# Kernel tuning notes

Measured on AMD Instinct MI355X. Metric: run time of the kernel, lower is better.

## Reference

```python
import jax, jax.numpy as jnp
import numpy as np

B, H, S, D = 2, 16, 2048, 64
MASK_NEG = 1e9


def setup_inputs() -> dict:
    key = jax.random.key(0)
    kq, kk, kv, km = jax.random.split(key, 4)
    Q = jax.random.normal(kq, (B, H, S, D), dtype=jnp.float32)
    K = jax.random.normal(kk, (B, H, S, D), dtype=jnp.float32)
    V = jax.random.normal(kv, (B, H, S, D), dtype=jnp.float32)
    # float 0/1 mask, broadcast over heads; 1 = masked-out position
    attn_mask = jax.random.randint(km, (B, 1, S, S), 0, 2).astype(jnp.float32)
    return {"Q": Q, "K": K, "V": V, "attn_mask": attn_mask}


def reference(Q, K, V, attn_mask):
    # scores: [B, H, S, S]
    attn_score = jnp.einsum('bhqd,bhkd->bhqk', Q, K)
    scale = jnp.sqrt(jnp.asarray(K.shape[-1], dtype=jnp.float32))
    attn_scale = attn_score / scale - MASK_NEG * attn_mask
    attn_prob = jax.nn.softmax(attn_scale, axis=-1)
    attn_out = jnp.einsum('bhqk,bhkd->bhqd', attn_prob, V)
    return attn_out
```

## Files before the change

kernel.cpp:

```cpp
#include <hip/hip_runtime.h>


#define S_LEN 2048
#define D_DIM 64
#define WPR   32
#define NIT   32

typedef __attribute__((ext_vector_type(8)))  short bf16x8;
typedef __attribute__((ext_vector_type(4)))  float f32x4;
typedef __attribute__((ext_vector_type(16))) float f32x16;
typedef unsigned uint2v __attribute__((ext_vector_type(2)));
typedef unsigned long long ull;

__device__ __forceinline__ f32x16 mfma32(bf16x8 a, bf16x8 b, f32x16 c) {
  return __builtin_amdgcn_mfma_f32_32x32x16_bf16(a, b, c, 0, 0, 0);
}
__device__ __forceinline__ f32x4 mfma16(bf16x8 a, bf16x8 b, f32x4 c) {
  return __builtin_amdgcn_mfma_f32_16x16x32_bf16(a, b, c, 0, 0, 0);
}
__device__ __forceinline__ unsigned short f2bf(float f) {
  unsigned u = __builtin_bit_cast(unsigned, f);
  unsigned r = u + 0x7FFFu + ((u >> 16) & 1u);
  return (unsigned short)(r >> 16);
}
__device__ __forceinline__ float bf2f(unsigned short s) {
  unsigned u = ((unsigned)s) << 16;
  return __builtin_bit_cast(float, u);
}
__device__ __forceinline__ unsigned packbf(float a, float b) {
  unsigned r;
  asm("v_cvt_pk_bf16_f32 %0, %1, %2" : "=v"(r) : "v"(a), "v"(b));
  return r;
}
__device__ __forceinline__ float fexp2(float x) {
#if __has_builtin(__builtin_amdgcn_exp2f)
  return __builtin_amdgcn_exp2f(x);
#else
  return exp2f(x);
#endif
}
__device__ __forceinline__ bool detect_bf16(const void* maskp) {
  const unsigned short* s = (const unsigned short*)maskp;
  unsigned short v = s[2 * (threadIdx.x & 63)];
  return __ballot(v == (unsigned short)0x3F80) != 0ull;
}
__device__ __forceinline__ int4 cvt_f8(const float* p) {
  float4 f0 = *(const float4*)p;
  float4 f1 = *(const float4*)(p + 4);
  int4 r;
  r.x = (int)packbf(f0.x, f0.y);
  r.y = (int)packbf(f0.z, f0.w);
  r.z = (int)packbf(f1.x, f1.y);
  r.w = (int)packbf(f1.z, f1.w);
  return r;
}

#define C1 0.18033688011112042f
#define C2 1.4426950408889634e9f

__global__ __launch_bounds__(256) void prep_all(
    const void* __restrict__ M, const void* __restrict__ Kin,
    const void* __restrict__ Vin, const void* __restrict__ Qin,
    ull* __restrict__ bits, unsigned short* __restrict__ Kf,
    unsigned short* __restrict__ Vf, unsigned short* __restrict__ Qc) {
  __shared__ __align__(16) unsigned short T[64 * 72];
  const bool isb = detect_bf16(M);
  const unsigned bx = blockIdx.x;
  const int tid = threadIdx.x;

  if (bx < 32768u) {
    unsigned idx = bx * 256u + tid;
    bool on = isb ? (bf2f(((const unsigned short*)M)[idx]) > 0.5f)
                  : (((const float*)M)[idx] > 0.5f);
    ull bm = __ballot(on);
    if ((tid & 63) == 0) {
      unsigned c = idx & 2047u, r = (idx >> 11) & 2047u, bb = idx >> 22;
      bits[(((size_t)(bb * WPR + (c >> 6))) << 11) + r] = bm;
    }
  } else if (bx < 32768u + 2048u) {
    unsigned g = (bx - 32768u) * 256u + tid;
    unsigned lane = g & 63u, f = (g >> 6) & 7u, it = (g >> 9) & 31u, bh = g >> 14;
    unsigned t = f >> 2, dc = f & 3, hi = lane >> 5, l31 = lane & 31;
    size_t src = (size_t)bh * (S_LEN * D_DIM) +
                 (size_t)(it * 64 + t * 32 + l31) * D_DIM + dc * 16 + hi * 8;
    int4 out;
    if (isb) out = *(const int4*)((const unsigned short*)Kin + src);
    else     out = cvt_f8((const float*)Kin + src);
    *(int4*)&Kf[(size_t)g * 8] = out;
  } else if (bx < 32768u + 2048u + 1024u) {
    unsigned idx = bx - (32768u + 2048u);
    unsigned bh = idx >> 5, it = idx & 31u;
    {
      int k = tid >> 2, d0 = (tid & 3) * 16;
      size_t src = (size_t)bh * (S_LEN * D_DIM) + (size_t)(it * 64 + k) * D_DIM + d0;
      int4 a, c;
      if (isb) {
        const unsigned short* s = (const unsigned short*)Vin + src;
        a = *(const int4*)s; c = *(const int4*)(s + 8);
      } else {
        const float* s = (const float*)Vin + src;
        a = cvt_f8(s); c = cvt_f8(s + 8);
      }
      *(int4*)&T[k * 72 + d0] = a;
      *(int4*)&T[k * 72 + d0 + 8] = c;
    }
    __syncthreads();
    #pragma unroll
    for (int h = 0; h < 2; ++h) {
      int c = tid + h * 256;
      int lane = c & 63, f = c >> 6;
      int t = f >> 2, kc = (f >> 1) & 1, dt = f & 1;
      int hi = lane >> 5, l31 = lane & 31;
      unsigned short v[8];
      #pragma unroll
      for (int j = 0; j < 8; ++j)
        v[j] = T[(t * 32 + kc * 16 + hi * 8 + j) * 72 + dt * 32 + l31];
      *(int4*)&Vf[(((size_t)(bh * 32 + it)) * 8 + f) * 512 + lane * 8] = *(int4*)v;
    }
  } else {
    size_t i0 = ((size_t)(bx - (32768u + 2048u + 1024u)) * 256 + tid) * 8;
    unsigned short v[8];
    if (isb) {
      *(int4*)v = *(const int4*)((const unsigned short*)Qin + i0);
      #pragma unroll
      for (int j = 0; j < 8; ++j) v[j] = f2bf(bf2f(v[j]) * C1);
    } else {
      const float* f = (const float*)Qin + i0;
      #pragma unroll
      for (int j = 0; j < 4; ++j)
        *((unsigned*)v + j) = packbf(f[2 * j] * C1, f[2 * j + 1] * C1);
    }
    *(int4*)&Qc[i0] = *(int4*)v;
  }
}

__global__ __launch_bounds__(256, 4) void attn_fast(
    const unsigned short* __restrict__ Qc, const unsigned short* __restrict__ Kf,
    const unsigned short* __restrict__ Vf, const ull* __restrict__ bits,
    const void* __restrict__ maskp, void* __restrict__ Op) {
  __shared__ float Comb[2][32][64];
  __shared__ float Lc[4][32];

  const bool isb = detect_bf16(maskp);
  const int tid  = threadIdx.x;
  const int wave = tid >> 6;
  const int lane = tid & 63;
  const int hi   = lane >> 5;
  const int l31  = lane & 31;
  const int id   = blockIdx.x;
  const int slot = id >> 3;
  const int bh   = (id & 7) * 4 + (slot & 3);
  const int q0   = (slot >> 2) * 32;
  const int b    = bh >> 4;
  const size_t base = (size_t)bh * S_LEN * D_DIM;
  const int xidx = ((lane ^ 32) & 63) * 4;

  bf16x8 qf[4];
  #pragma unroll
  for (int dc = 0; dc < 4; ++dc)
    qf[dc] = *(const bf16x8*)&Qc[base + (size_t)(q0 + l31) * D_DIM + dc * 16 + hi * 8];

  f32x16 acc_o[2];
  float ls0 = 0.f, ls1 = 0.f, ls2 = 0.f, ls3 = 0.f;
  #pragma unroll
  for (int r = 0; r < 16; ++r) { acc_o[0][r] = 0.f; acc_o[1][r] = 0.f; }

  for (int i = 0; i < NIT / 4; ++i) {
    const int it = wave * (NIT / 4) + i;
    const size_t fb = ((size_t)(bh * 32 + it)) * 8 * 512;

    ull w = bits[(((size_t)(b * WPR + it)) << 11) + q0 + l31] >> (hi * 4);
    unsigned wt[2] = {(unsigned)w, (unsigned)(w >> 32)};

    #pragma unroll
    for (int t = 0; t < 2; ++t) {
      const unsigned short* Kb = Kf + fb + (size_t)(t * 4) * 512 + lane * 8;
      f32x16 sc;
      #pragma unroll
      for (int r = 0; r < 16; ++r) sc[r] = 0.f;
      #pragma unroll
      for (int dc = 0; dc < 4; ++dc) {
        bf16x8 kfr = *(const bf16x8*)(Kb + dc * 512);
        sc = mfma32(kfr, qf[dc], sc);
      }

      float p[16];
      #pragma unroll
      for (int r = 0; r < 16; ++r) {
        float e = fexp2(sc[r]);
        unsigned bit = (wt[t] >> ((r & 3) + 8 * (r >> 2))) & 1u;
        p[r] = bit ? 0.0f : e;
      }
      ls0 += p[0] + p[4] + p[8]  + p[12];
      ls1 += p[1] + p[5] + p[9]  + p[13];
      ls2 += p[2] + p[6] + p[10] + p[14];
      ls3 += p[3] + p[7] + p[11] + p[15];

      #pragma unroll
      for (int kc = 0; kc < 2; ++kc) {
        unsigned pk0 = packbf(p[8 * kc + 0], p[8 * kc + 1]);
        unsigned pk1 = packbf(p[8 * kc + 2], p[8 * kc + 3]);
        unsigned pk2 = packbf(p[8 * kc + 4], p[8 * kc + 5]);
        unsigned pk3 = packbf(p[8 * kc + 6], p[8 * kc + 7]);
        uint4 d;
#if __has_builtin(__builtin_amdgcn_permlane32_swap)
        uint2v s02 = __builtin_amdgcn_permlane32_swap(pk0, pk2, false, false);
        uint2v s13 = __builtin_amdgcn_permlane32_swap(pk1, pk3, false, false);
        d.x = s02[0]; d.z = s02[1];
        d.y = s13[0]; d.w = s13[1];
#else
        unsigned x0 = (unsigned)__builtin_amdgcn_ds_bpermute(xidx, (int)pk0);
        unsigned x1 = (unsigned)__builtin_amdgcn_ds_bpermute(xidx, (int)pk1);
        unsigned x2 = (unsigned)__builtin_amdgcn_ds_bpermute(xidx, (int)pk2);
        unsigned x3 = (unsigned)__builtin_amdgcn_ds_bpermute(xidx, (int)pk3);
        d.x = hi ? x2 : pk0;
        d.y = hi ? x3 : pk1;
        d.z = hi ? pk2 : x0;
        d.w = hi ? pk3 : x1;
#endif
        bf16x8 pf = __builtin_bit_cast(bf16x8, d);

        const unsigned short* Vb = Vf + fb + (size_t)(t * 4 + kc * 2) * 512 + lane * 8;
        #pragma unroll
        for (int dt = 0; dt < 2; ++dt) {
          bf16x8 vfr = *(const bf16x8*)(Vb + dt * 512);
          acc_o[dt] = mfma32(pf, vfr, acc_o[dt]);
        }
      }
    }
  }

  float lsum = (ls0 + ls1) + (ls2 + ls3);
  {
    int li = __builtin_bit_cast(int, lsum);
    float other = __builtin_bit_cast(float, __builtin_amdgcn_ds_bpermute(xidx, li));
    lsum += other;
  }

  __syncthreads();
  if (wave >= 2) {
    #pragma unroll
    for (int dt = 0; dt < 2; ++dt)
      #pragma unroll
      for (int r = 0; r < 16; ++r)
        Comb[wave - 2][dt * 16 + r][lane] = acc_o[dt][r];
  }
  if (hi == 0) Lc[wave][l31] = lsum;
  __syncthreads();
  if (wave < 2) {
    #pragma unroll
    for (int dt = 0; dt < 2; ++dt)
      #pragma unroll
      for (int r = 0; r < 16; ++r)
        acc_o[dt][r] += Comb[wave][dt * 16 + r][lane];
  }
  __syncthreads();
  if (wave == 1) {
    #pragma unroll
    for (int dt = 0; dt < 2; ++dt)
      #pragma unroll
      for (int r = 0; r < 16; ++r)
        Comb[0][dt * 16 + r][lane] = acc_o[dt][r];
  }
  __syncthreads();
  if (wave == 0) {
    #pragma unroll
    for (int r = 0; r < 16; ++r) {
      int m = (r & 3) + 8 * (r >> 2) + 4 * hi;
      float o0 = acc_o[0][r] + Comb[0][r][lane];
      float o1 = acc_o[1][r] + Comb[0][16 + r][lane];
      float lv = Lc[0][m] + Lc[1][m] + Lc[2][m] + Lc[3][m];
      float inv = 1.0f / lv;
      size_t idx = base + (size_t)(q0 + m) * D_DIM + l31;
      if (isb) {
        ((unsigned short*)Op)[idx]      = f2bf(o0 * inv);
        ((unsigned short*)Op)[idx + 32] = f2bf(o1 * inv);
      } else {
        ((float*)Op)[idx]      = o0 * inv;
        ((float*)Op)[idx + 32] = o1 * inv;
      }
    }
  }
}

__global__ __launch_bounds__(256, 2) void attn_fallback(
    const void* __restrict__ Qp, const void* __restrict__ Kp,
    const void* __restrict__ Vp, const void* __restrict__ maskp,
    void* __restrict__ Op) {
  __shared__ __align__(16) short QKlds[128 * 72];
  __shared__ __align__(16) short Vtlds[64 * 72];
  __shared__ __align__(16) short Plds2[128 * 72];

  const bool isb = detect_bf16(maskp);
  const int tid  = threadIdx.x;
  const int wave = tid >> 6;
  const int lane = tid & 63;
  const int l15  = lane & 15;
  const int quad = lane >> 4;
  const int q0   = blockIdx.x * 128;
  const int bh   = blockIdx.y;
  const int b    = bh >> 4;
  const size_t base = (size_t)bh * S_LEN * D_DIM;

  const short* Qs = (const short*)Qp; const float* Qf = (const float*)Qp;
  const short* Ks = (const short*)Kp; const float* Kf2 = (const float*)Kp;
  const short* Vs = (const short*)Vp; const float* Vf2 = (const float*)Vp;

  if (isb) {
    const short* Qg = Qs + base + (size_t)q0 * D_DIM;
    #pragma unroll
    for (int p = 0; p < 4; ++p) {
      int e = p * 2048 + tid * 8;
      *(int4*)&QKlds[(e >> 6) * 72 + (e & 63)] = *(const int4*)(Qg + e);
    }
  } else {
    const float* Qg = Qf + base + (size_t)q0 * D_DIM;
    #pragma unroll
    for (int p = 0; p < 4; ++p) {
      int e = p * 2048 + tid * 8;
      *(int4*)&QKlds[(e >> 6) * 72 + (e & 63)] = cvt_f8(Qg + e);
    }
  }
  __syncthreads();
  bf16x8 qf[2][2];
  #pragma unroll
  for (int mi = 0; mi < 2; ++mi)
    #pragma unroll
    for (int kt = 0; kt < 2; ++kt)
      qf[mi][kt] = *(const bf16x8*)&QKlds[(wave * 32 + mi * 16 + l15) * 72 + kt * 32 + quad * 8];
  __syncthreads();

  f32x4 acc_o[2][4];
  f32x4 acc_l[2];
  const f32x4 zero4 = {0.f, 0.f, 0.f, 0.f};
  #pragma unroll
  for (int mi = 0; mi < 2; ++mi) {
    acc_l[mi] = zero4;
    #pragma unroll
    for (int nt = 0; nt < 4; ++nt) acc_o[mi][nt] = zero4;
  }
  bf16x8 onesB;
  {
    short ov = (l15 == 0) ? (short)0x3F80 : (short)0;
    #pragma unroll
    for (int i = 0; i < 8; ++i) onesB[i] = ov;
  }

  for (int it = 0; it < NIT; ++it) {
    const int k0 = it * 64;
    if (isb) {
      const short* Kg = Ks + base + (size_t)k0 * D_DIM;
      #pragma unroll
      for (int p = 0; p < 2; ++p) {
        int e = p * 2048 + tid * 8;
        *(int4*)&QKlds[(e >> 6) * 72 + (e & 63)] = *(const int4*)(Kg + e);
      }
    } else {
      const float* Kg = Kf2 + base + (size_t)k0 * D_DIM;
      #pragma unroll
      for (int p = 0; p < 2; ++p) {
        int e = p * 2048 + tid * 8;
        *(int4*)&QKlds[(e >> 6) * 72 + (e & 63)] = cvt_f8(Kg + e);
      }
    }
    {
      const int r0 = (tid >> 3) * 2;
      const int d0 = (tid & 7) * 8;
      unsigned short as_[8], bs_[8];
      if (isb) {
        const short* Vg = Vs + base + (size_t)k0 * D_DIM;
        *(int4*)as_ = *(const int4*)(Vg + r0 * D_DIM + d0);
        *(int4*)bs_ = *(const int4*)(Vg + (r0 + 1) * D_DIM + d0);
      } else {
        const float* Vg = Vf2 + base + (size_t)k0 * D_DIM;
        *(int4*)as_ = cvt_f8(Vg + r0 * D_DIM + d0);
        *(int4*)bs_ = cvt_f8(Vg + (r0 + 1) * D_DIM + d0);
      }
      #pragma unroll
      for (int j = 0; j < 8; ++j) {
        int d = d0 + j;
        int blk = (r0 >> 3) ^ (d >> 3);
        unsigned pk = (unsigned)as_[j] | ((unsigned)bs_[j] << 16);
        *(unsigned*)&Vtlds[d * 72 + blk * 8 + (r0 & 7)] = pk;
      }
    }
    __syncthreads();

    f32x4 sc[2][4];
    #pragma unroll
    for (int mi = 0; mi < 2; ++mi)
      #pragma unroll
      for (int nt = 0; nt < 4; ++nt) sc[mi][nt] = zero4;
    #pragma unroll
    for (int nt = 0; nt < 4; ++nt) {
      bf16x8 kf0 = *(const bf16x8*)&QKlds[(nt * 16 + l15) * 72 + quad * 8];
      bf16x8 kf1 = *(const bf16x8*)&QKlds[(nt * 16 + l15) * 72 + 32 + quad * 8];
      #pragma unroll
      for (int mi = 0; mi < 2; ++mi) {
        sc[mi][nt] = mfma16(qf[mi][0], kf0, sc[mi][nt]);
        sc[mi][nt] = mfma16(qf[mi][1], kf1, sc[mi][nt]);
      }
    }

    #pragma unroll
    for (int mi = 0; mi < 2; ++mi) {
      #pragma unroll
      for (int nt = 0; nt < 4; ++nt) {
        #pragma unroll
        for (int reg = 0; reg < 4; ++reg) {
          int rg = q0 + wave * 32 + mi * 16 + quad * 4 + reg;
          size_t mix = (size_t)b * S_LEN * S_LEN + (size_t)rg * S_LEN + k0 + nt * 16 + l15;
          float mv = isb ? bf2f(((const unsigned short*)maskp)[mix])
                         : ((const float*)maskp)[mix];
          float y = sc[mi][nt][reg] * C1 - mv * C2;
          Plds2[(wave * 32 + mi * 16 + quad * 4 + reg) * 72 + nt * 16 + l15] =
              (short)f2bf(fexp2(y));
        }
      }
    }
    __syncthreads();

    #pragma unroll
    for (int kt = 0; kt < 2; ++kt) {
      bf16x8 pf[2];
      #pragma unroll
      for (int mi = 0; mi < 2; ++mi)
        pf[mi] = *(const bf16x8*)&Plds2[(wave * 32 + mi * 16 + l15) * 72 + kt * 32 + quad * 8];
      #pragma unroll
      for (int nt = 0; nt < 4; ++nt) {
        int d = nt * 16 + l15;
        int kb = (kt * 4 + quad) ^ (d >> 3);
        bf16x8 vf = *(const bf16x8*)&Vtlds[d * 72 + kb * 8];
        #pragma unroll
        for (int mi = 0; mi < 2; ++mi)
          acc_o[mi][nt] = mfma16(pf[mi], vf, acc_o[mi][nt]);
      }
      #pragma unroll
      for (int mi = 0; mi < 2; ++mi)
        acc_l[mi] = mfma16(pf[mi], onesB, acc_l[mi]);
    }
    __syncthreads();
  }

  #pragma unroll
  for (int mi = 0; mi < 2; ++mi) {
    #pragma unroll
    for (int reg = 0; reg < 4; ++reg) {
      float lv = __shfl(acc_l[mi][reg], lane & 48, 64);
      float inv = 1.0f / lv;
      #pragma unroll
      for (int nt = 0; nt < 4; ++nt) {
        float o = acc_o[mi][nt][reg] * inv;
        size_t idx = base + (size_t)(q0 + wave * 32 + mi * 16 + quad * 4 + reg) * D_DIM + nt * 16 + l15;
        if (isb) ((unsigned short*)Op)[idx] = f2bf(o);
        else     ((float*)Op)[idx] = o;
      }
    }
  }
}

extern "C" void kernel_launch(void* const* d_in, const int* in_sizes, int n_in,
                              void* d_out, int out_size, void* d_ws, size_t ws_size,
                              hipStream_t stream) {
  const void* Q = d_in[0];
  const void* K = d_in[1];
  const void* V = d_in[2];
  const void* M = d_in[3];

  dim3 block(256);
  const size_t bits_bytes = (size_t)2 * S_LEN * S_LEN / 8;
  const size_t tens_bytes = (size_t)2 * 16 * S_LEN * D_DIM * 2;

  if (ws_size >= bits_bytes + 3 * tens_bytes) {
    char* ws = (char*)d_ws;
    ull* bits = (ull*)ws;
    unsigned short* Kf = (unsigned short*)(ws + bits_bytes);
    unsigned short* Vf = (unsigned short*)(ws + bits_bytes + tens_bytes);
    unsigned short* Qc = (unsigned short*)(ws + bits_bytes + 2 * tens_bytes);
    prep_all<<<dim3(32768 + 2048 + 1024 + 2048), block, 0, stream>>>(
        M, K, V, Q, bits, Kf, Vf, Qc);
    attn_fast<<<dim3(2048), block, 0, stream>>>(Qc, Kf, Vf, bits, M, d_out);
  } else {
    attn_fallback<<<dim3(S_LEN / 128, 32), block, 0, stream>>>(Q, K, V, M, d_out);
  }
}
```

Before: 186.2 us.

## Software-pipeline K/V/mask loads in attention loop and batch mask packing per block

The attention main loop is fully unrolled into 16 steps. Each step prefetches the next K fragments and mask word while computing the current tile, and V fragments are loaded before the score MFMAs, so memory latency overlaps with compute. Separately, the mask-to-bitmask prep now has each block process 8 chunks of 256 elements, cutting the grid from 32768 to 4096 blocks for that segment. Both raise register pressure and code size, which could hurt occupancy under the 4-waves launch bound.

```diff
diff --git a/kernel.cpp b/kernel.cpp
--- a/kernel.cpp
+++ b/kernel.cpp
@@ -58,6 +58,11 @@
 #define C1 0.18033688011112042f
 #define C2 1.4426950408889634e9f
 
+#define SEG0 4096u
+#define SEG1 2048u
+#define SEG2 1024u
+#define SEG3 2048u
+
 __global__ __launch_bounds__(256) void prep_all(
     const void* __restrict__ M, const void* __restrict__ Kin,
     const void* __restrict__ Vin, const void* __restrict__ Qin,
@@ -68,17 +73,21 @@
   const unsigned bx = blockIdx.x;
   const int tid = threadIdx.x;
 
-  if (bx < 32768u) {
-    unsigned idx = bx * 256u + tid;
-    bool on = isb ? (bf2f(((const unsigned short*)M)[idx]) > 0.5f)
-                  : (((const float*)M)[idx] > 0.5f);
-    ull bm = __ballot(on);
-    if ((tid & 63) == 0) {
-      unsigned c = idx & 2047u, r = (idx >> 11) & 2047u, bb = idx >> 22;
-      bits[(((size_t)(bb * WPR + (c >> 6))) << 11) + r] = bm;
-    }
-  } else if (bx < 32768u + 2048u) {
-    unsigned g = (bx - 32768u) * 256u + tid;
+  if (bx < SEG0) {
+    unsigned e0 = bx * 2048u + tid;
+    #pragma unroll
+    for (int j = 0; j < 8; ++j) {
+      unsigned idx = e0 + (unsigned)j * 256u;
+      bool on = isb ? (bf2f(((const unsigned short*)M)[idx]) > 0.5f)
+                    : (((const float*)M)[idx] > 0.5f);
+      ull bm = __ballot(on);
+      if ((tid & 63) == 0) {
+        unsigned c = idx & 2047u, r = (idx >> 11) & 2047u, bb = idx >> 22;
+        bits[(((size_t)(bb * WPR + (c >> 6))) << 11) + r] = bm;
+      }
+    }
+  } else if (bx < SEG0 + SEG1) {
+    unsigned g = (bx - SEG0) * 256u + tid;
     unsigned lane = g & 63u, f = (g >> 6) & 7u, it = (g >> 9) & 31u, bh = g >> 14;
     unsigned t = f >> 2, dc = f & 3, hi = lane >> 5, l31 = lane & 31;
     size_t src = (size_t)bh * (S_LEN * D_DIM) +
@@ -87,8 +96,8 @@
     if (isb) out = *(const int4*)((const unsigned short*)Kin + src);
     else     out = cvt_f8((const float*)Kin + src);
     *(int4*)&Kf[(size_t)g * 8] = out;
-  } else if (bx < 32768u + 2048u + 1024u) {
-    unsigned idx = bx - (32768u + 2048u);
+  } else if (bx < SEG0 + SEG1 + SEG2) {
+    unsigned idx = bx - (SEG0 + SEG1);
     unsigned bh = idx >> 5, it = idx & 31u;
     {
       int k = tid >> 2, d0 = (tid & 3) * 16;
@@ -118,7 +127,7 @@
       *(int4*)&Vf[(((size_t)(bh * 32 + it)) * 8 + f) * 512 + lane * 8] = *(int4*)v;
     }
   } else {
-    size_t i0 = ((size_t)(bx - (32768u + 2048u + 1024u)) * 256 + tid) * 8;
+    size_t i0 = ((size_t)(bx - (SEG0 + SEG1 + SEG2)) * 256 + tid) * 8;
     unsigned short v[8];
     if (isb) {
       *(int4*)v = *(const int4*)((const unsigned short*)Qin + i0);
@@ -160,74 +169,92 @@
   for (int dc = 0; dc < 4; ++dc)
     qf[dc] = *(const bf16x8*)&Qc[base + (size_t)(q0 + l31) * D_DIM + dc * 16 + hi * 8];
 
+  const unsigned short* KbBase = Kf + ((size_t)(bh * 32 + wave * 8) * 8) * 512 + lane * 8;
+  const unsigned short* VbBase = Vf + ((size_t)(bh * 32 + wave * 8) * 8) * 512 + lane * 8;
+  const size_t bitrow = ((size_t)(b * WPR + wave * 8) << 11) + q0 + l31;
+
   f32x16 acc_o[2];
   float ls0 = 0.f, ls1 = 0.f, ls2 = 0.f, ls3 = 0.f;
   #pragma unroll
   for (int r = 0; r < 16; ++r) { acc_o[0][r] = 0.f; acc_o[1][r] = 0.f; }
 
-  for (int i = 0; i < NIT / 4; ++i) {
-    const int it = wave * (NIT / 4) + i;
-    const size_t fb = ((size_t)(bh * 32 + it)) * 8 * 512;
-
-    ull w = bits[(((size_t)(b * WPR + it)) << 11) + q0 + l31] >> (hi * 4);
-    unsigned wt[2] = {(unsigned)w, (unsigned)(w >> 32)};
-
-    #pragma unroll
-    for (int t = 0; t < 2; ++t) {
-      const unsigned short* Kb = Kf + fb + (size_t)(t * 4) * 512 + lane * 8;
-      f32x16 sc;
-      #pragma unroll
-      for (int r = 0; r < 16; ++r) sc[r] = 0.f;
-      #pragma unroll
-      for (int dc = 0; dc < 4; ++dc) {
-        bf16x8 kfr = *(const bf16x8*)(Kb + dc * 512);
-        sc = mfma32(kfr, qf[dc], sc);
-      }
-
-      float p[16];
-      #pragma unroll
-      for (int r = 0; r < 16; ++r) {
-        float e = fexp2(sc[r]);
-        unsigned bit = (wt[t] >> ((r & 3) + 8 * (r >> 2))) & 1u;
-        p[r] = bit ? 0.0f : e;
-      }
-      ls0 += p[0] + p[4] + p[8]  + p[12];
-      ls1 += p[1] + p[5] + p[9]  + p[13];
-      ls2 += p[2] + p[6] + p[10] + p[14];
-      ls3 += p[3] + p[7] + p[11] + p[15];
-
-      #pragma unroll
-      for (int kc = 0; kc < 2; ++kc) {
-        unsigned pk0 = packbf(p[8 * kc + 0], p[8 * kc + 1]);
-        unsigned pk1 = packbf(p[8 * kc + 2], p[8 * kc + 3]);
-        unsigned pk2 = packbf(p[8 * kc + 4], p[8 * kc + 5]);
-        unsigned pk3 = packbf(p[8 * kc + 6], p[8 * kc + 7]);
-        uint4 d;
+  bf16x8 ka[4];
+  #pragma unroll
+  for (int dc = 0; dc < 4; ++dc)
+    ka[dc] = *(const bf16x8*)(KbBase + (size_t)dc * 512);
+  ull wcur = bits[bitrow];
+
+  #pragma unroll
+  for (int tt = 0; tt < 16; ++tt) {
+    const int i = tt >> 1, t = tt & 1;
+    const int off = i * 8 + t * 4;
+
+    bf16x8 kn[4];
+    if (tt < 15) {
+      #pragma unroll
+      for (int dc = 0; dc < 4; ++dc)
+        kn[dc] = *(const bf16x8*)(KbBase + (size_t)(off + 4 + dc) * 512);
+    }
+    ull wnext = wcur;
+    if (t == 1 && i < 7) wnext = bits[bitrow + ((size_t)(i + 1) << 11)];
+    bf16x8 vv[4];
+    #pragma unroll
+    for (int f = 0; f < 4; ++f)
+      vv[f] = *(const bf16x8*)(VbBase + (size_t)(off + f) * 512);
+
+    f32x16 sc;
+    #pragma unroll
+    for (int r = 0; r < 16; ++r) sc[r] = 0.f;
+    #pragma unroll
+    for (int dc = 0; dc < 4; ++dc) sc = mfma32(ka[dc], qf[dc], sc);
+
+    const unsigned wtv = (unsigned)((wcur >> (hi * 4)) >> (32 * t));
+
+    float p[16];
+    #pragma unroll
+    for (int r = 0; r < 16; ++r) {
+      float e = fexp2(sc[r]);
+      unsigned bit = (wtv >> ((r & 3) + 8 * (r >> 2))) & 1u;
+      p[r] = bit ? 0.0f : e;
+    }
+    ls0 += p[0] + p[4] + p[8]  + p[12];
+    ls1 += p[1] + p[5] + p[9]  + p[13];
+    ls2 += p[2] + p[6] + p[10] + p[14];
+    ls3 += p[3] + p[7] + p[11] + p[15];
+
+    #pragma unroll
+    for (int kc = 0; kc < 2; ++kc) {
+      unsigned pk0 = packbf(p[8 * kc + 0], p[8 * kc + 1]);
+      unsigned pk1 = packbf(p[8 * kc + 2], p[8 * kc + 3]);
+      unsigned pk2 = packbf(p[8 * kc + 4], p[8 * kc + 5]);
+      unsigned pk3 = packbf(p[8 * kc + 6], p[8 * kc + 7]);
+      uint4 d;
 #if __has_builtin(__builtin_amdgcn_permlane32_swap)
-        uint2v s02 = __builtin_amdgcn_permlane32_swap(pk0, pk2, false, false);
-        uint2v s13 = __builtin_amdgcn_permlane32_swap(pk1, pk3, false, false);
-        d.x = s02[0]; d.z = s02[1];
-        d.y = s13[0]; d.w = s13[1];
+      uint2v s02 = __builtin_amdgcn_permlane32_swap(pk0, pk2, false, false);
+      uint2v s13 = __builtin_amdgcn_permlane32_swap(pk1, pk3, false, false);
+      d.x = s02[0]; d.z = s02[1];
+      d.y = s13[0]; d.w = s13[1];
 #else
-        unsigned x0 = (unsigned)__builtin_amdgcn_ds_bpermute(xidx, (int)pk0);
-        unsigned x1 = (unsigned)__builtin_amdgcn_ds_bpermute(xidx, (int)pk1);
-        unsigned x2 = (unsigned)__builtin_amdgcn_ds_bpermute(xidx, (int)pk2);
-        unsigned x3 = (unsigned)__builtin_amdgcn_ds_bpermute(xidx, (int)pk3);
-        d.x = hi ? x2 : pk0;
-        d.y = hi ? x3 : pk1;
-        d.z = hi ? pk2 : x0;
-        d.w = hi ? pk3 : x1;
+      unsigned x0 = (unsigned)__builtin_amdgcn_ds_bpermute(xidx, (int)pk0);
+      unsigned x1 = (unsigned)__builtin_amdgcn_ds_bpermute(xidx, (int)pk1);
+      unsigned x2 = (unsigned)__builtin_amdgcn_ds_bpermute(xidx, (int)pk2);
+      unsigned x3 = (unsigned)__builtin_amdgcn_ds_bpermute(xidx, (int)pk3);
+      d.x = hi ? x2 : pk0;
+      d.y = hi ? x3 : pk1;
+      d.z = hi ? pk2 : x0;
+      d.w = hi ? pk3 : x1;
 #endif
-        bf16x8 pf = __builtin_bit_cast(bf16x8, d);
-
-        const unsigned short* Vb = Vf + fb + (size_t)(t * 4 + kc * 2) * 512 + lane * 8;
-        #pragma unroll
-        for (int dt = 0; dt < 2; ++dt) {
-          bf16x8 vfr = *(const bf16x8*)(Vb + dt * 512);
-          acc_o[dt] = mfma32(pf, vfr, acc_o[dt]);
-        }
-      }
-    }
+      bf16x8 pf = __builtin_bit_cast(bf16x8, d);
+      #pragma unroll
+      for (int dt = 0; dt < 2; ++dt)
+        acc_o[dt] = mfma32(pf, vv[kc * 2 + dt], acc_o[dt]);
+    }
+
+    if (tt < 15) {
+      #pragma unroll
+      for (int dc = 0; dc < 4; ++dc) ka[dc] = kn[dc];
+    }
+    if (t == 1) wcur = wnext;
   }
 
   float lsum = (ls0 + ls1) + (ls2 + ls3);
@@ -477,7 +504,7 @@
     unsigned short* Kf = (unsigned short*)(ws + bits_bytes);
     unsigned short* Vf = (unsigned short*)(ws + bits_bytes + tens_bytes);
     unsigned short* Qc = (unsigned short*)(ws + bits_bytes + 2 * tens_bytes);
-    prep_all<<<dim3(32768 + 2048 + 1024 + 2048), block, 0, stream>>>(
+    prep_all<<<dim3(SEG0 + SEG1 + SEG2 + SEG3), block, 0, stream>>>(
         M, K, V, Q, bits, Kf, Vf, Qc);
     attn_fast<<<dim3(2048), block, 0, stream>>>(Qc, Kf, Vf, bits, M, d_out);
   } else {
```

New measurement: 212.9 us. +14.3%, slower.

## Share K/V tiles across four query waves via LDS double-buffered async loads

Applied to the files above, without the earlier changes.

Before, each block split the key range across its four waves for a single 32-row query tile and then reduced the partial outputs through shared memory. Now each wave owns its own 32-row query tile (128 queries per block) and walks all 64 key steps. K/V fragments are staged once per block into a double-buffered LDS area with global_load_lds and reused by all four waves. This cuts redundant K/V global traffic and removes the cross-wave combine, at the cost of a block barrier every key step and a quarter as many blocks (512). The mask-packing prep blocks also each handle eight ballots instead of one, shrinking the prep grid.

```diff
diff --git a/kernel.cpp b/kernel.cpp
--- a/kernel.cpp
+++ b/kernel.cpp
@@ -54,9 +54,23 @@
   r.w = (int)packbf(f1.z, f1.w);
   return r;
 }
+__device__ __forceinline__ void gl_lds16(const unsigned short* g, unsigned short* l) {
+#if __has_builtin(__builtin_amdgcn_global_load_lds)
+  __builtin_amdgcn_global_load_lds(
+      (const __attribute__((address_space(1))) unsigned int*)g,
+      (__attribute__((address_space(3))) unsigned int*)l, 16, 0, 0);
+#else
+  *(int4*)((char*)l + (threadIdx.x & 63) * 16) = *(const int4*)g;
+#endif
+}
 
 #define C1 0.18033688011112042f
 #define C2 1.4426950408889634e9f
+
+#define SEG0 4096u
+#define SEG1 2048u
+#define SEG2 1024u
+#define SEG3 2048u
 
 __global__ __launch_bounds__(256) void prep_all(
     const void* __restrict__ M, const void* __restrict__ Kin,
@@ -68,17 +82,21 @@
   const unsigned bx = blockIdx.x;
   const int tid = threadIdx.x;
 
-  if (bx < 32768u) {
-    unsigned idx = bx * 256u + tid;
-    bool on = isb ? (bf2f(((const unsigned short*)M)[idx]) > 0.5f)
-                  : (((const float*)M)[idx] > 0.5f);
-    ull bm = __ballot(on);
-    if ((tid & 63) == 0) {
-      unsigned c = idx & 2047u, r = (idx >> 11) & 2047u, bb = idx >> 22;
-      bits[(((size_t)(bb * WPR + (c >> 6))) << 11) + r] = bm;
-    }
-  } else if (bx < 32768u + 2048u) {
-    unsigned g = (bx - 32768u) * 256u + tid;
+  if (bx < SEG0) {
+    unsigned e0 = bx * 2048u + tid;
+    #pragma unroll
+    for (int j = 0; j < 8; ++j) {
+      unsigned idx = e0 + (unsigned)j * 256u;
+      bool on = isb ? (bf2f(((const unsigned short*)M)[idx]) > 0.5f)
+                    : (((const float*)M)[idx] > 0.5f);
+      ull bm = __ballot(on);
+      if ((tid & 63) == 0) {
+        unsigned c = idx & 2047u, r = (idx >> 11) & 2047u, bb = idx >> 22;
+        bits[(((size_t)(bb * WPR + (c >> 6))) << 11) + r] = bm;
+      }
+    }
+  } else if (bx < SEG0 + SEG1) {
+    unsigned g = (bx - SEG0) * 256u + tid;
     unsigned lane = g & 63u, f = (g >> 6) & 7u, it = (g >> 9) & 31u, bh = g >> 14;
     unsigned t = f >> 2, dc = f & 3, hi = lane >> 5, l31 = lane & 31;
     size_t src = (size_t)bh * (S_LEN * D_DIM) +
@@ -87,8 +105,8 @@
     if (isb) out = *(const int4*)((const unsigned short*)Kin + src);
     else     out = cvt_f8((const float*)Kin + src);
     *(int4*)&Kf[(size_t)g * 8] = out;
-  } else if (bx < 32768u + 2048u + 1024u) {
-    unsigned idx = bx - (32768u + 2048u);
+  } else if (bx < SEG0 + SEG1 + SEG2) {
+    unsigned idx = bx - (SEG0 + SEG1);
     unsigned bh = idx >> 5, it = idx & 31u;
     {
       int k = tid >> 2, d0 = (tid & 3) * 16;
@@ -118,7 +136,7 @@
       *(int4*)&Vf[(((size_t)(bh * 32 + it)) * 8 + f) * 512 + lane * 8] = *(int4*)v;
     }
   } else {
-    size_t i0 = ((size_t)(bx - (32768u + 2048u + 1024u)) * 256 + tid) * 8;
+    size_t i0 = ((size_t)(bx - (SEG0 + SEG1 + SEG2)) * 256 + tid) * 8;
     unsigned short v[8];
     if (isb) {
       *(int4*)v = *(const int4*)((const unsigned short*)Qin + i0);
@@ -138,8 +156,8 @@
     const unsigned short* __restrict__ Qc, const unsigned short* __restrict__ Kf,
     const unsigned short* __restrict__ Vf, const ull* __restrict__ bits,
     const void* __restrict__ maskp, void* __restrict__ Op) {
-  __shared__ float Comb[2][32][64];
-  __shared__ float Lc[4][32];
+  __shared__ __align__(16) unsigned short Stg[2][8][512];
+  __shared__ float Ls[4][32];
 
   const bool isb = detect_bf16(maskp);
   const int tid  = threadIdx.x;
@@ -150,7 +168,8 @@
   const int id   = blockIdx.x;
   const int slot = id >> 3;
   const int bh   = (id & 7) * 4 + (slot & 3);
-  const int q0   = (slot >> 2) * 32;
+  const int qb   = slot >> 2;
+  const int qbase = qb * 128 + wave * 32;
   const int b    = bh >> 4;
   const size_t base = (size_t)bh * S_LEN * D_DIM;
   const int xidx = ((lane ^ 32) & 63) * 4;
@@ -158,76 +177,85 @@
   bf16x8 qf[4];
   #pragma unroll
   for (int dc = 0; dc < 4; ++dc)
-    qf[dc] = *(const bf16x8*)&Qc[base + (size_t)(q0 + l31) * D_DIM + dc * 16 + hi * 8];
+    qf[dc] = *(const bf16x8*)&Qc[base + (size_t)(qbase + l31) * D_DIM + dc * 16 + hi * 8];
+
+  const unsigned short* Ksrc = Kf + (size_t)bh * 131072 + (size_t)wave * 512 + lane * 8;
+  const unsigned short* Vsrc = Vf + (size_t)bh * 131072 + (size_t)wave * 512 + lane * 8;
+  const size_t bitbase = ((size_t)(b * WPR) << 11) + (size_t)(qbase + l31);
 
   f32x16 acc_o[2];
   float ls0 = 0.f, ls1 = 0.f, ls2 = 0.f, ls3 = 0.f;
   #pragma unroll
   for (int r = 0; r < 16; ++r) { acc_o[0][r] = 0.f; acc_o[1][r] = 0.f; }
 
-  for (int i = 0; i < NIT / 4; ++i) {
-    const int it = wave * (NIT / 4) + i;
-    const size_t fb = ((size_t)(bh * 32 + it)) * 8 * 512;
-
-    ull w = bits[(((size_t)(b * WPR + it)) << 11) + q0 + l31] >> (hi * 4);
-    unsigned wt[2] = {(unsigned)w, (unsigned)(w >> 32)};
-
-    #pragma unroll
-    for (int t = 0; t < 2; ++t) {
-      const unsigned short* Kb = Kf + fb + (size_t)(t * 4) * 512 + lane * 8;
-      f32x16 sc;
-      #pragma unroll
-      for (int r = 0; r < 16; ++r) sc[r] = 0.f;
-      #pragma unroll
-      for (int dc = 0; dc < 4; ++dc) {
-        bf16x8 kfr = *(const bf16x8*)(Kb + dc * 512);
-        sc = mfma32(kfr, qf[dc], sc);
-      }
-
-      float p[16];
-      #pragma unroll
-      for (int r = 0; r < 16; ++r) {
-        float e = fexp2(sc[r]);
-        unsigned bit = (wt[t] >> ((r & 3) + 8 * (r >> 2))) & 1u;
-        p[r] = bit ? 0.0f : e;
-      }
-      ls0 += p[0] + p[4] + p[8]  + p[12];
-      ls1 += p[1] + p[5] + p[9]  + p[13];
-      ls2 += p[2] + p[6] + p[10] + p[14];
-      ls3 += p[3] + p[7] + p[11] + p[15];
-
-      #pragma unroll
-      for (int kc = 0; kc < 2; ++kc) {
-        unsigned pk0 = packbf(p[8 * kc + 0], p[8 * kc + 1]);
-        unsigned pk1 = packbf(p[8 * kc + 2], p[8 * kc + 3]);
-        unsigned pk2 = packbf(p[8 * kc + 4], p[8 * kc + 5]);
-        unsigned pk3 = packbf(p[8 * kc + 6], p[8 * kc + 7]);
-        uint4 d;
+  gl_lds16(Ksrc, &Stg[0][wave][0]);
+  gl_lds16(Vsrc, &Stg[0][4 + wave][0]);
+  __syncthreads();
+
+  ull wcur = 0;
+  #pragma unroll 2
+  for (int ks = 0; ks < 64; ++ks) {
+    const int cur = ks & 1;
+    if (ks < 63) {
+      gl_lds16(Ksrc + (size_t)(ks + 1) * 2048, &Stg[cur ^ 1][wave][0]);
+      gl_lds16(Vsrc + (size_t)(ks + 1) * 2048, &Stg[cur ^ 1][4 + wave][0]);
+    }
+    if (!(ks & 1)) wcur = bits[bitbase + ((size_t)(ks >> 1) << 11)];
+
+    f32x16 sc;
+    #pragma unroll
+    for (int r = 0; r < 16; ++r) sc[r] = 0.f;
+    #pragma unroll
+    for (int dc = 0; dc < 4; ++dc) {
+      bf16x8 kfr = *(const bf16x8*)&Stg[cur][dc][lane * 8];
+      sc = mfma32(kfr, qf[dc], sc);
+    }
+
+    const unsigned wtv = (unsigned)((wcur >> (hi * 4)) >> (32 * (ks & 1)));
+
+    float p[16];
+    #pragma unroll
+    for (int r = 0; r < 16; ++r) {
+      float e = fexp2(sc[r]);
+      unsigned bit = (wtv >> ((r & 3) + 8 * (r >> 2))) & 1u;
+      p[r] = bit ? 0.0f : e;
+    }
+    ls0 += p[0] + p[4] + p[8]  + p[12];
+    ls1 += p[1] + p[5] + p[9]  + p[13];
+    ls2 += p[2] + p[6] + p[10] + p[14];
+    ls3 += p[3] + p[7] + p[11] + p[15];
+
+    #pragma unroll
+    for (int kc = 0; kc < 2; ++kc) {
+      unsigned pk0 = packbf(p[8 * kc + 0], p[8 * kc + 1]);
+      unsigned pk1 = packbf(p[8 * kc + 2], p[8 * kc + 3]);
+      unsigned pk2 = packbf(p[8 * kc + 4], p[8 * kc + 5]);
+      unsigned pk3 = packbf(p[8 * kc + 6], p[8 * kc + 7]);
+      uint4 d;
 #if __has_builtin(__builtin_amdgcn_permlane32_swap)
-        uint2v s02 = __builtin_amdgcn_permlane32_swap(pk0, pk2, false, false);
-        uint2v s13 = __builtin_amdgcn_permlane32_swap(pk1, pk3, false, false);
-        d.x = s02[0]; d.z = s02[1];
-        d.y = s13[0]; d.w = s13[1];
+      uint2v s02 = __builtin_amdgcn_permlane32_swap(pk0, pk2, false, false);
+      uint2v s13 = __builtin_amdgcn_permlane32_swap(pk1, pk3, false, false);
+      d.x = s02[0]; d.z = s02[1];
+      d.y = s13[0]; d.w = s13[1];
 #else
-        unsigned x0 = (unsigned)__builtin_amdgcn_ds_bpermute(xidx, (int)pk0);
-        unsigned x1 = (unsigned)__builtin_amdgcn_ds_bpermute(xidx, (int)pk1);
-        unsigned x2 = (unsigned)__builtin_amdgcn_ds_bpermute(xidx, (int)pk2);
-        unsigned x3 = (unsigned)__builtin_amdgcn_ds_bpermute(xidx, (int)pk3);
-        d.x = hi ? x2 : pk0;
-        d.y = hi ? x3 : pk1;
-        d.z = hi ? pk2 : x0;
-        d.w = hi ? pk3 : x1;
+      unsigned x0 = (unsigned)__builtin_amdgcn_ds_bpermute(xidx, (int)pk0);
+      unsigned x1 = (unsigned)__builtin_amdgcn_ds_bpermute(xidx, (int)pk1);
+      unsigned x2 = (unsigned)__builtin_amdgcn_ds_bpermute(xidx, (int)pk2);
+      unsigned x3 = (unsigned)__builtin_amdgcn_ds_bpermute(xidx, (int)pk3);
+      d.x = hi ? x2 : pk0;
+      d.y = hi ? x3 : pk1;
+      d.z = hi ? pk2 : x0;
+      d.w = hi ? pk3 : x1;
 #endif
-        bf16x8 pf = __builtin_bit_cast(bf16x8, d);
-
-        const unsigned short* Vb = Vf + fb + (size_t)(t * 4 + kc * 2) * 512 + lane * 8;
-        #pragma unroll
-        for (int dt = 0; dt < 2; ++dt) {
-          bf16x8 vfr = *(const bf16x8*)(Vb + dt * 512);
-          acc_o[dt] = mfma32(pf, vfr, acc_o[dt]);
-        }
-      }
-    }
+      bf16x8 pf = __builtin_bit_cast(bf16x8, d);
+      #pragma unroll
+      for (int dt = 0; dt < 2; ++dt) {
+        bf16x8 vfr = *(const bf16x8*)&Stg[cur][4 + kc * 2 + dt][lane * 8];
+        acc_o[dt] = mfma32(pf, vfr, acc_o[dt]);
+      }
+    }
+
+    __syncthreads();
   }
 
   float lsum = (ls0 + ls1) + (ls2 + ls3);
@@ -236,49 +264,21 @@
     float other = __builtin_bit_cast(float, __builtin_amdgcn_ds_bpermute(xidx, li));
     lsum += other;
   }
-
-  __syncthreads();
-  if (wave >= 2) {
-    #pragma unroll
-    for (int dt = 0; dt < 2; ++dt)
-      #pragma unroll
-      for (int r = 0; r < 16; ++r)
-        Comb[wave - 2][dt * 16 + r][lane] = acc_o[dt][r];
-  }
-  if (hi == 0) Lc[wave][l31] = lsum;
-  __syncthreads();
-  if (wave < 2) {
-    #pragma unroll
-    for (int dt = 0; dt < 2; ++dt)
-      #pragma unroll
-      for (int r = 0; r < 16; ++r)
-        acc_o[dt][r] += Comb[wave][dt * 16 + r][lane];
-  }
-  __syncthreads();
-  if (wave == 1) {
-    #pragma unroll
-    for (int dt = 0; dt < 2; ++dt)
-      #pragma unroll
-      for (int r = 0; r < 16; ++r)
-        Comb[0][dt * 16 + r][lane] = acc_o[dt][r];
-  }
-  __syncthreads();
-  if (wave == 0) {
-    #pragma unroll
-    for (int r = 0; r < 16; ++r) {
-      int m = (r & 3) + 8 * (r >> 2) + 4 * hi;
-      float o0 = acc_o[0][r] + Comb[0][r][lane];
-      float o1 = acc_o[1][r] + Comb[0][16 + r][lane];
-      float lv = Lc[0][m] + Lc[1][m] + Lc[2][m] + Lc[3][m];
-      float inv = 1.0f / lv;
-      size_t idx = base + (size_t)(q0 + m) * D_DIM + l31;
-      if (isb) {
-        ((unsigned short*)Op)[idx]      = f2bf(o0 * inv);
-        ((unsigned short*)Op)[idx + 32] = f2bf(o1 * inv);
-      } else {
-        ((float*)Op)[idx]      = o0 * inv;
-        ((float*)Op)[idx + 32] = o1 * inv;
-      }
+  if (hi == 0) Ls[wave][l31] = lsum;
+
+  #pragma unroll
+  for (int r = 0; r < 16; ++r) {
+    int m = (r & 3) + 8 * (r >> 2) + 4 * hi;
+    float inv = 1.0f / Ls[wave][m];
+    float o0 = acc_o[0][r] * inv;
+    float o1 = acc_o[1][r] * inv;
+    size_t idx = base + (size_t)(qbase + m) * D_DIM + l31;
+    if (isb) {
+      ((unsigned short*)Op)[idx]      = f2bf(o0);
+      ((unsigned short*)Op)[idx + 32] = f2bf(o1);
+    } else {
+      ((float*)Op)[idx]      = o0;
+      ((float*)Op)[idx + 32] = o1;
     }
   }
 }
@@ -477,9 +477,9 @@
     unsigned short* Kf = (unsigned short*)(ws + bits_bytes);
     unsigned short* Vf = (unsigned short*)(ws + bits_bytes + tens_bytes);
     unsigned short* Qc = (unsigned short*)(ws + bits_bytes + 2 * tens_bytes);
-    prep_all<<<dim3(32768 + 2048 + 1024 + 2048), block, 0, stream>>>(
+    prep_all<<<dim3(SEG0 + SEG1 + SEG2 + SEG3), block, 0, stream>>>(
         M, K, V, Q, bits, Kf, Vf, Qc);
-    attn_fast<<<dim3(2048), block, 0, stream>>>(Qc, Kf, Vf, bits, M, d_out);
+    attn_fast<<<dim3(512), block, 0, stream>>>(Qc, Kf, Vf, bits, M, d_out);
   } else {
     attn_fallback<<<dim3(S_LEN / 128, 32), block, 0, stream>>>(Q, K, V, M, d_out);
   }
```

Result: faster. 172.5 us (-7.3%).
